# Performance work log

Measured on AMD Instinct MI355X. Metric: run time of the kernel, lower is better.

The kernel has to match this reference:

```python
import math
import jax, jax.numpy as jnp
import numpy as np

B = 8
S = 1024  # equal per-sequence length -> cu_seqlens = arange(B+1)*S
H = 16
D = 64


def setup_inputs() -> dict:
    key = jax.random.key(0)
    kq, kk, kv = jax.random.split(key, 3)
    T = B * S
    q = jax.random.normal(kq, (T, H, D), dtype=jnp.float32)
    k = jax.random.normal(kk, (T, H, D), dtype=jnp.float32)
    v = jax.random.normal(kv, (T, H, D), dtype=jnp.float32)
    cu_seqlens = (jnp.arange(B + 1, dtype=jnp.int32) * S)
    return {"q": q, "k": k, "v": v, "cu_seqlens": cu_seqlens, "max_seqlen": S}


def reference(q, k, v, cu_seqlens, max_seqlen):
    # Non-causal varlen attention over packed sequences.
    # q, k, v: [total_tokens, H, D]; cu_seqlens: [B+1] int32.
    # Sequences here are equal-length, so the packed layout reshapes to [B,S,H,D];
    # a cu_seqlens-derived validity mask keeps the math identical to the varlen kernel.
    T, h, d = q.shape
    b = cu_seqlens.shape[0] - 1
    s = T // b
    scale = 1.0 / math.sqrt(d)

    seq_lens = cu_seqlens[1:] - cu_seqlens[:-1]            # [b]
    valid = jnp.arange(s)[None, :] < seq_lens[:, None]      # [b, s] bool

    qb = q.reshape(b, s, h, d)
    kb = k.reshape(b, s, h, d)
    vb = v.reshape(b, s, h, d)

    scores = jnp.einsum("bqhd,bkhd->bhqk", qb, kb) * scale  # [b,h,s,s]
    neg = jnp.asarray(-1e30, dtype=scores.dtype)
    scores = jnp.where(valid[:, None, None, :], scores, neg)
    p = jax.nn.softmax(scores, axis=-1)
    out = jnp.einsum("bhqk,bkhd->bqhd", p, vb)              # [b,s,h,d]
    out = jnp.where(valid[:, :, None, None], out, 0.0)
    return out.reshape(T, h, d)
```

## Files before the change

### kernel.cpp

```cpp
#include <hip/hip_runtime.h>

#define H_DIM 16
#define D_DIM 64
#define QBLK 256
#define KVBLK 64
#define NTHREADS 512
#define TOKSTRIDE (H_DIM * D_DIM)

typedef __bf16 bf16x8 __attribute__((ext_vector_type(8)));
typedef float  f32x4  __attribute__((ext_vector_type(4)));

__global__ __launch_bounds__(NTHREADS, 4)
void attn_fwd(const float* __restrict__ qg, const float* __restrict__ kg,
              const float* __restrict__ vg, const int* __restrict__ cu,
              float* __restrict__ out, int tiles)
{
    __shared__ __align__(16) __bf16 Klds[2][KVBLK * D_DIM];
    __shared__ __align__(16) __bf16 Vlds[2][KVBLK * D_DIM];

    int nwg = gridDim.x;
    int bid = blockIdx.x;
    int lg = ((nwg & 7) == 0) ? ((bid & 7) * (nwg >> 3) + (bid >> 3)) : bid;

    int qt  = lg % tiles;
    int sh  = lg / tiles;
    int h   = sh % H_DIM;
    int seq = sh / H_DIM;

    int cu0 = cu[seq], cu1 = cu[seq + 1];
    int len = cu1 - cu0;
    int q0  = qt * QBLK;
    if (len <= 0 || q0 >= len) return;

    int tid  = threadIdx.x;
    int wid  = tid >> 6;
    int lane = tid & 63;
    int g    = lane >> 4;
    int c    = lane & 15;

    const float SC = 0.125f * 1.44269504088896340736f;

    bf16x8 qf[2][2];
    #pragma unroll
    for (int rg = 0; rg < 2; ++rg) {
        int qrow = q0 + wid * 32 + rg * 16 + c;
        bool valid = qrow < len;
        const float* qp = qg + ((cu0 + qrow) * TOKSTRIDE + h * D_DIM);
        #pragma unroll
        for (int ks = 0; ks < 2; ++ks) {
            float4 a = valid ? *(const float4*)(qp + ks * 32 + g * 8)     : make_float4(0,0,0,0);
            float4 b = valid ? *(const float4*)(qp + ks * 32 + g * 8 + 4) : make_float4(0,0,0,0);
            qf[rg][ks][0] = (__bf16)(a.x * SC); qf[rg][ks][1] = (__bf16)(a.y * SC);
            qf[rg][ks][2] = (__bf16)(a.z * SC); qf[rg][ks][3] = (__bf16)(a.w * SC);
            qf[rg][ks][4] = (__bf16)(b.x * SC); qf[rg][ks][5] = (__bf16)(b.y * SC);
            qf[rg][ks][6] = (__bf16)(b.z * SC); qf[rg][ks][7] = (__bf16)(b.w * SC);
        }
    }

    f32x4 o0[4] = {}, o1[4] = {};
    float l0 = 0.0f, l1 = 0.0f;

    int krow = tid >> 3;
    int kc   = tid & 7;
    int kwoff = krow * 128 + ((kc * 16) ^ ((krow & 7) << 4));
    int vfg  = tid >> 6;
    int vd   = tid & 63;
    int vr0  = 32 * (vfg >> 2) + 4 * (vfg & 3);

    const float* kptr = kg + (cu0 + krow) * TOKSTRIDE + h * D_DIM + kc * 8;
    const float* vptr = vg + (cu0 + vr0)  * TOKSTRIDE + h * D_DIM + vd;

    float4 ka, kb;
    float  vv[8];

    auto do_load = [&](int kb0) {
        if (kb0 + KVBLK <= len) {
            ka = *(const float4*)kptr;
            kb = *(const float4*)(kptr + 4);
            #pragma unroll
            for (int i = 0; i < 8; ++i)
                vv[i] = vptr[(i >> 2) * (16 * TOKSTRIDE) + (i & 3) * TOKSTRIDE];
        } else {
            if (kb0 + krow < len) {
                ka = *(const float4*)kptr;
                kb = *(const float4*)(kptr + 4);
            } else {
                ka = make_float4(0,0,0,0); kb = make_float4(0,0,0,0);
            }
            #pragma unroll
            for (int i = 0; i < 8; ++i) {
                int r = kb0 + vr0 + 16 * (i >> 2) + (i & 3);
                vv[i] = (r < len) ? vptr[(i >> 2) * (16 * TOKSTRIDE) + (i & 3) * TOKSTRIDE] : 0.f;
            }
        }
        kptr += KVBLK * TOKSTRIDE;
        vptr += KVBLK * TOKSTRIDE;
    };
    auto write_tile = [&](int buf) {
        bf16x8 kw;
        kw[0]=(__bf16)ka.x; kw[1]=(__bf16)ka.y; kw[2]=(__bf16)ka.z; kw[3]=(__bf16)ka.w;
        kw[4]=(__bf16)kb.x; kw[5]=(__bf16)kb.y; kw[6]=(__bf16)kb.z; kw[7]=(__bf16)kb.w;
        *(bf16x8*)((char*)Klds[buf] + kwoff) = kw;
        bf16x8 vw;
        #pragma unroll
        for (int i = 0; i < 8; ++i) vw[i] = (__bf16)vv[i];
        *(bf16x8*)(Vlds[buf] + (tid << 3)) = vw;
    };

    int nkv = (len + KVBLK - 1) / KVBLK;

    do_load(0);
    write_tile(0);
    __syncthreads();

    int cur = 0;
    for (int kt = 0; kt < nkv; ++kt) {
        int kbase = kt * KVBLK;
        bool more = kt + 1 < nkv;
        if (more) do_load(kbase + KVBLK);

        const __bf16* K = Klds[cur];
        f32x4 s0[4] = {}, s1[4] = {};
        __builtin_amdgcn_s_setprio(1);
        #pragma unroll
        for (int b = 0; b < 4; ++b) {
            int rowk = 16 * b + c;
            int swz = (rowk & 7) << 4;
            const char* base = (const char*)K + rowk * 128;
            bf16x8 a0 = *(const bf16x8*)(base + ((16 * g)      ^ swz));
            bf16x8 a1 = *(const bf16x8*)(base + ((64 + 16 * g) ^ swz));
            s0[b] = __builtin_amdgcn_mfma_f32_16x16x32_bf16(a0, qf[0][0], s0[b], 0, 0, 0);
            s0[b] = __builtin_amdgcn_mfma_f32_16x16x32_bf16(a1, qf[0][1], s0[b], 0, 0, 0);
            s1[b] = __builtin_amdgcn_mfma_f32_16x16x32_bf16(a0, qf[1][0], s1[b], 0, 0, 0);
            s1[b] = __builtin_amdgcn_mfma_f32_16x16x32_bf16(a1, qf[1][1], s1[b], 0, 0, 0);
        }
        __builtin_amdgcn_s_setprio(0);

        if (kbase + KVBLK > len) {
            #pragma unroll
            for (int b = 0; b < 4; ++b)
                #pragma unroll
                for (int r = 0; r < 4; ++r)
                    if (kbase + 16 * b + 4 * g + r >= len) { s0[b][r] = -3.0e38f; s1[b][r] = -3.0e38f; }
        }

        bf16x8 p0[2], p1[2];
        float ps0 = 0.f, ps1 = 0.f;
        #pragma unroll
        for (int M = 0; M < 2; ++M)
            #pragma unroll
            for (int i = 0; i < 8; ++i) {
                float e0 = __builtin_amdgcn_exp2f(s0[2 * M + (i >> 2)][i & 3]);
                float e1 = __builtin_amdgcn_exp2f(s1[2 * M + (i >> 2)][i & 3]);
                p0[M][i] = (__bf16)e0; p1[M][i] = (__bf16)e1;
                ps0 += e0; ps1 += e1;
            }
        l0 += ps0; l1 += ps1;

        const __bf16* V = Vlds[cur];
        __builtin_amdgcn_s_setprio(1);
        #pragma unroll
        for (int nb = 0; nb < 4; ++nb) {
            #pragma unroll
            for (int M = 0; M < 2; ++M) {
                bf16x8 vf = *(const bf16x8*)(V + ((((M << 2) + g) << 6) + (nb << 4) + c) * 8);
                o0[nb] = __builtin_amdgcn_mfma_f32_16x16x32_bf16(p0[M], vf, o0[nb], 0, 0, 0);
                o1[nb] = __builtin_amdgcn_mfma_f32_16x16x32_bf16(p1[M], vf, o1[nb], 0, 0, 0);
            }
        }
        __builtin_amdgcn_s_setprio(0);

        if (more) write_tile(cur ^ 1);
        __syncthreads();
        cur ^= 1;
    }

    l0 += __shfl_xor(l0, 16);  l0 += __shfl_xor(l0, 32);
    l1 += __shfl_xor(l1, 16);  l1 += __shfl_xor(l1, 32);

    #pragma unroll
    for (int r = 0; r < 4; ++r) {
        float lr0 = __shfl(l0, 4 * g + r);
        float lr1 = __shfl(l1, 4 * g + r);
        float li0 = (lr0 > 0.f) ? 1.0f / lr0 : 0.f;
        float li1 = (lr1 > 0.f) ? 1.0f / lr1 : 0.f;
        int qrowA = q0 + wid * 32 + 4 * g + r;
        int qrowB = qrowA + 16;
        if (qrowA < len) {
            float* op = out + ((cu0 + qrowA) * TOKSTRIDE + h * D_DIM);
            #pragma unroll
            for (int nb = 0; nb < 4; ++nb) op[nb * 16 + c] = o0[nb][r] * li0;
        }
        if (qrowB < len) {
            float* op = out + ((cu0 + qrowB) * TOKSTRIDE + h * D_DIM);
            #pragma unroll
            for (int nb = 0; nb < 4; ++nb) op[nb * 16 + c] = o1[nb][r] * li1;
        }
    }
}

extern "C" void kernel_launch(void* const* d_in, const int* in_sizes, int n_in,
                              void* d_out, int out_size, void* d_ws, size_t ws_size,
                              hipStream_t stream) {
    const float* q  = (const float*)d_in[0];
    const float* k  = (const float*)d_in[1];
    const float* v  = (const float*)d_in[2];
    const int*   cu = (const int*)d_in[3];

    int nseq  = in_sizes[3] - 1;
    int T     = in_sizes[0] / (H_DIM * D_DIM);
    int S     = T / nseq;
    int tiles = (S + QBLK - 1) / QBLK;
    int nwg   = nseq * H_DIM * tiles;

    attn_fwd<<<nwg, NTHREADS, 0, stream>>>(q, k, v, cu, (float*)d_out, tiles);
}
```

Baseline: 57.17 us.

## Double Q tile to 512 rows with 1024 threads sharing each KV tile

Measured after the change: 56.22 us. Within noise of the previous version (-1.7%).

```diff
diff --git a/kernel.cpp b/kernel.cpp
--- a/kernel.cpp
+++ b/kernel.cpp
@@ -2,12 +2,13 @@
 
 #define H_DIM 16
 #define D_DIM 64
-#define QBLK 256
+#define QBLK 512
 #define KVBLK 64
-#define NTHREADS 512
+#define NTHREADS 1024
 #define TOKSTRIDE (H_DIM * D_DIM)
 
 typedef __bf16 bf16x8 __attribute__((ext_vector_type(8)));
+typedef __bf16 bf16x4 __attribute__((ext_vector_type(4)));
 typedef float  f32x4  __attribute__((ext_vector_type(4)));
 
 __global__ __launch_bounds__(NTHREADS, 4)
@@ -60,51 +61,48 @@
     f32x4 o0[4] = {}, o1[4] = {};
     float l0 = 0.0f, l1 = 0.0f;
 
-    int krow = tid >> 3;
-    int kc   = tid & 7;
-    int kwoff = krow * 128 + ((kc * 16) ^ ((krow & 7) << 4));
-    int vfg  = tid >> 6;
-    int vd   = tid & 63;
-    int vr0  = 32 * (vfg >> 2) + 4 * (vfg & 3);
-
-    const float* kptr = kg + (cu0 + krow) * TOKSTRIDE + h * D_DIM + kc * 8;
-    const float* vptr = vg + (cu0 + vr0)  * TOKSTRIDE + h * D_DIM + vd;
-
-    float4 ka, kb;
-    float  vv[8];
+    int krow = tid >> 4;
+    int kc   = tid & 15;
+    int kwoff = krow * 128 + ((((kc >> 1) * 16) ^ ((krow & 7) << 4)) + (kc & 1) * 8);
+    int vf_  = tid >> 1;
+    int vhal = tid & 1;
+    int vfg  = vf_ >> 6;
+    int vd   = vf_ & 63;
+    int vbase = 32 * (vfg >> 2) + 16 * vhal + 4 * (vfg & 3);
+
+    const float* kptr = kg + (cu0 + krow)  * TOKSTRIDE + h * D_DIM + kc * 4;
+    const float* vptr = vg + (cu0 + vbase) * TOKSTRIDE + h * D_DIM + vd;
+
+    bf16x4 kst, vst;
 
     auto do_load = [&](int kb0) {
         if (kb0 + KVBLK <= len) {
-            ka = *(const float4*)kptr;
-            kb = *(const float4*)(kptr + 4);
-            #pragma unroll
-            for (int i = 0; i < 8; ++i)
-                vv[i] = vptr[(i >> 2) * (16 * TOKSTRIDE) + (i & 3) * TOKSTRIDE];
+            float4 f4 = *(const float4*)kptr;
+            kst[0] = (__bf16)f4.x; kst[1] = (__bf16)f4.y;
+            kst[2] = (__bf16)f4.z; kst[3] = (__bf16)f4.w;
+            #pragma unroll
+            for (int j = 0; j < 4; ++j)
+                vst[j] = (__bf16)vptr[j * TOKSTRIDE];
         } else {
             if (kb0 + krow < len) {
-                ka = *(const float4*)kptr;
-                kb = *(const float4*)(kptr + 4);
+                float4 f4 = *(const float4*)kptr;
+                kst[0] = (__bf16)f4.x; kst[1] = (__bf16)f4.y;
+                kst[2] = (__bf16)f4.z; kst[3] = (__bf16)f4.w;
             } else {
-                ka = make_float4(0,0,0,0); kb = make_float4(0,0,0,0);
-            }
-            #pragma unroll
-            for (int i = 0; i < 8; ++i) {
-                int r = kb0 + vr0 + 16 * (i >> 2) + (i & 3);
-                vv[i] = (r < len) ? vptr[(i >> 2) * (16 * TOKSTRIDE) + (i & 3) * TOKSTRIDE] : 0.f;
+                kst[0] = kst[1] = kst[2] = kst[3] = (__bf16)0.0f;
+            }
+            #pragma unroll
+            for (int j = 0; j < 4; ++j) {
+                int r = kb0 + vbase + j;
+                vst[j] = (r < len) ? (__bf16)vptr[j * TOKSTRIDE] : (__bf16)0.0f;
             }
         }
         kptr += KVBLK * TOKSTRIDE;
         vptr += KVBLK * TOKSTRIDE;
     };
     auto write_tile = [&](int buf) {
-        bf16x8 kw;
-        kw[0]=(__bf16)ka.x; kw[1]=(__bf16)ka.y; kw[2]=(__bf16)ka.z; kw[3]=(__bf16)ka.w;
-        kw[4]=(__bf16)kb.x; kw[5]=(__bf16)kb.y; kw[6]=(__bf16)kb.z; kw[7]=(__bf16)kb.w;
-        *(bf16x8*)((char*)Klds[buf] + kwoff) = kw;
-        bf16x8 vw;
-        #pragma unroll
-        for (int i = 0; i < 8; ++i) vw[i] = (__bf16)vv[i];
-        *(bf16x8*)(Vlds[buf] + (tid << 3)) = vw;
+        *(bf16x4*)((char*)Klds[buf] + kwoff) = kst;
+        *(bf16x4*)((char*)Vlds[buf] + (tid << 3)) = vst;
     };
 
     int nkv = (len + KVBLK - 1) / KVBLK;
```
